# Performance work log

Hardware: AMD Instinct MI355X
Metric: run time of the kernel (lower is better)

Reference implementation:

```python
import jax, jax.numpy as jnp
import numpy as np

HIDDEN = 256


def _lstm_cell(x, h, c, W_ih, W_hh, b_ih, b_hh):
    # torch.nn.LSTMCell: gates ordered [i, f, g, o], gates = x W_ih^T + h W_hh^T + b_ih + b_hh
    gates = x @ W_ih.T + h @ W_hh.T + (b_ih + b_hh)
    i, f, g, o = jnp.split(gates, 4, axis=-1)
    c_new = jax.nn.sigmoid(f) * c + jax.nn.sigmoid(i) * jnp.tanh(g)
    h_new = jax.nn.sigmoid(o) * jnp.tanh(c_new)
    return h_new, c_new


def setup_inputs() -> dict:
    key = jax.random.key(0)
    ks = jax.random.split(key, 16)
    s = 1.0 / np.sqrt(HIDDEN)  # torch LSTMCell init scale
    inp = {
        "tracks": jax.random.normal(ks[0], (256, 512, 2), dtype=jnp.float32),
        "W_ih0": jax.random.uniform(ks[1], (1024, 2), jnp.float32, -s, s),
        "W_hh0": jax.random.uniform(ks[2], (1024, 256), jnp.float32, -s, s),
        "b_ih0": jax.random.uniform(ks[3], (1024,), jnp.float32, -s, s),
        "b_hh0": jax.random.uniform(ks[4], (1024,), jnp.float32, -s, s),
        "W_ih1": jax.random.uniform(ks[5], (1024, 256), jnp.float32, -s, s),
        "W_hh1": jax.random.uniform(ks[6], (1024, 256), jnp.float32, -s, s),
        "b_ih1": jax.random.uniform(ks[7], (1024,), jnp.float32, -s, s),
        "b_hh1": jax.random.uniform(ks[8], (1024,), jnp.float32, -s, s),
        "W_ih2": jax.random.uniform(ks[9], (1024, 256), jnp.float32, -s, s),
        "W_hh2": jax.random.uniform(ks[10], (1024, 256), jnp.float32, -s, s),
        "b_ih2": jax.random.uniform(ks[11], (1024,), jnp.float32, -s, s),
        "b_hh2": jax.random.uniform(ks[12], (1024,), jnp.float32, -s, s),
        "W_pred": jax.random.uniform(ks[13], (2, 256), jnp.float32, -s, s),
        "b_pred": jax.random.uniform(ks[14], (2,), jnp.float32, -s, s),
    }
    return inp


def reference(tracks, W_ih0, W_hh0, b_ih0, b_hh0, W_ih1, W_hh1, b_ih1, b_hh1,
              W_ih2, W_hh2, b_ih2, b_hh2, W_pred, b_pred):
    B = tracks.shape[0]
    layers = [(W_ih0, W_hh0, b_ih0, b_hh0),
              (W_ih1, W_hh1, b_ih1, b_hh1),
              (W_ih2, W_hh2, b_ih2, b_hh2)]
    zeros = jnp.zeros((B, HIDDEN), dtype=tracks.dtype)
    init_carry = tuple((zeros, zeros) for _ in layers)

    def step(carry, x_t):
        new_carry = []
        h = x_t
        for (hc, params) in zip(carry, layers):
            h, c = _lstm_cell(h, hc[0], hc[1], *params)
            new_carry.append((h, c))
        return tuple(new_carry), None

    xs = jnp.swapaxes(tracks, 0, 1)  # [T, B, 2]
    final_carry, _ = jax.lax.scan(step, init_carry, xs)
    h = final_carry[-1][0]  # last layer's final hidden state
    h = jax.nn.elu(h)
    return h @ W_pred.T + b_pred
```

## Files before the change

kernel.cpp:

```cpp
#include <hip/hip_runtime.h>
#include <math.h>

typedef __attribute__((ext_vector_type(4))) float f32x4;
typedef __attribute__((ext_vector_type(4))) int   i32x4;
typedef __attribute__((ext_vector_type(8))) short bfrag8;

#define WRE_LO_OFF 2621440
#define HB_OFF     5242880
#define TAG_OFF    6815744
#define HSTRIDE    65536

#define WROW 264
#define SMEM_BYTES (4 * 64 * WROW * 2)

__device__ __forceinline__ unsigned short f2bf(float f){
  union { float f; unsigned u; } x; x.f = f;
  unsigned r = x.u + 0x7FFFu + ((x.u >> 16) & 1u);
  return (unsigned short)(r >> 16);
}
__device__ __forceinline__ float bf2f(unsigned short s){
  union { unsigned u; float f; } x; x.u = ((unsigned)s) << 16; return x.f;
}
__device__ __forceinline__ float sigf(float x){
  return 1.0f / (1.0f + __expf(-x));
}
__device__ __forceinline__ float tanh_fast(float x){
  x = fminf(fmaxf(x, -15.0f), 15.0f);
  float e = __expf(2.0f * x);
  return (e - 1.0f) / (e + 1.0f);
}

__device__ __forceinline__ i32x4 llc_load_b128(const void* p){
  i32x4 r;
  asm volatile("global_load_dwordx4 %0, %1, off sc0 sc1"
               : "=v"(r) : "v"(p) : "memory");
  return r;
}
__device__ __forceinline__ void llc_store_b16(void* p, unsigned short v){
  unsigned int vv = v;
  asm volatile("global_store_short %0, %1, off sc0 sc1"
               : : "v"(p), "v"(vv) : "memory");
}
__device__ __forceinline__ void wait_vm0(){
  asm volatile("s_waitcnt vmcnt(0)" ::: "memory");
}

__global__ void init_reorder(const float* __restrict__ hh0, const float* __restrict__ ih1,
                             const float* __restrict__ hh1, const float* __restrict__ ih2,
                             const float* __restrict__ hh2,
                             unsigned short* __restrict__ wre_hi,
                             unsigned short* __restrict__ wre_lo){
  int e = blockIdx.x * 256 + threadIdx.x;
  int mat = e >> 18;
  int d   = (e >> 8) & 1023;
  int k   = e & 255;
  int nt = d >> 6, g = (d >> 4) & 3, n = d & 15;
  int src_row = g*256 + nt*16 + n;
  const float* W = (mat==0) ? hh0 : (mat==1) ? ih1 : (mat==2) ? hh1 : (mat==3) ? ih2 : hh2;
  float v = W[src_row*256 + k];
  unsigned short hi = f2bf(v);
  float lo = v - bf2f(hi);
  wre_hi[e] = hi;
  wre_lo[e] = f2bf(lo);
}

__global__ void init_zero(uint4* __restrict__ p, int n16){
  int i = blockIdx.x * 256 + threadIdx.x;
  if (i < n16) p[i] = make_uint4(0u,0u,0u,0u);
}

__global__ void init_tags(unsigned int* __restrict__ tags){
  int i = blockIdx.x * 256 + threadIdx.x;
  if (i < 3072) tags[i] = (unsigned)(i / 768);
}

__global__ void __launch_bounds__(256, 1) lstm_coop(
    const float* __restrict__ tracks,
    const float* __restrict__ wih0,
    const float* __restrict__ bih0, const float* __restrict__ bhh0,
    const float* __restrict__ bih1, const float* __restrict__ bhh1,
    const float* __restrict__ bih2, const float* __restrict__ bhh2,
    const unsigned short* __restrict__ wre_hi, const unsigned short* __restrict__ wre_lo,
    unsigned short* __restrict__ hb, unsigned int* __restrict__ tags);

template<int L>
__device__ __forceinline__ void layer_loop(
    const float* __restrict__ tracks, const float* __restrict__ wih0,
    const float* __restrict__ bihL, const float* __restrict__ bhhL,
    const unsigned short* smem,
    unsigned short* hb, unsigned int* tags,
    int nt, int bt)
{
  const int tid  = threadIdx.x;
  const int w    = tid >> 6, lane = tid & 63;
  const int m    = lane & 15, q = lane >> 4;
  const int b0   = bt * 64, n0 = nt * 16;
  const int G    = bt * 4 + w;

  float bsum[4], wx0[4], wx1[4];
  #pragma unroll
  for (int g = 0; g < 4; ++g){
    int row = g*256 + n0 + m;
    bsum[g] = bihL[row] + bhhL[row];
    if constexpr (L == 0){ wx0[g] = wih0[row*2 + 0]; wx1[g] = wih0[row*2 + 1]; }
  }
  float cst[4] = {0.f, 0.f, 0.f, 0.f};
  const int arow = b0 + 16*w + m;
  const int woff = m*WROW + q*8;
  constexpr int RS = (L == 0) ? 0 : 2;

  for (int t = 0; t < 512; ++t){
    const int pin  = t & 3;
    const int prec = (t + 3) & 3;
    const unsigned expi = (unsigned)(t + 4);
    const unsigned expr = (unsigned)(t + 3);

    unsigned gv = 0u;
    unsigned int* gl = nullptr;
    if constexpr (L < 2){
      gl = tags + ((pin*3 + (L+1))*16 + G)*16;
      if (lane < 16)
        gv = __hip_atomic_load(gl + lane, __ATOMIC_RELAXED, __HIP_MEMORY_SCOPE_AGENT);
    }

    float xv0[4], xv1[4];
    if constexpr (L == 0){
      #pragma unroll
      for (int r = 0; r < 4; ++r){
        const float* px = tracks + (b0 + 16*w + q*4 + r)*1024 + t*2;
        xv0[r] = px[0]; xv1[r] = px[1];
      }
    }

    unsigned int* rcl = tags + ((prec*3 + L)*16 + G)*16;
    unsigned int* inl = nullptr;
    if constexpr (L >= 1) inl = tags + ((pin*3 + (L-1))*16 + G)*16;
    for (;;){
      bool ok = true;
      if constexpr (L >= 1){
        if (lane < 16)
          ok = __hip_atomic_load(inl + lane, __ATOMIC_RELAXED, __HIP_MEMORY_SCOPE_AGENT) >= expi;
        else if (lane < 32)
          ok = __hip_atomic_load(rcl + (lane - 16), __ATOMIC_RELAXED, __HIP_MEMORY_SCOPE_AGENT) >= expr;
      } else {
        if (lane < 16)
          ok = __hip_atomic_load(rcl + lane, __ATOMIC_RELAXED, __HIP_MEMORY_SCOPE_AGENT) >= expr;
      }
      if (__all((int)ok)) break;
    }

    i32x4 arr[8], ari[8];
    {
      const unsigned short* pr = hb + (prec*3 + L)*HSTRIDE + arow*256 + q*8;
      #pragma unroll
      for (int ks = 0; ks < 8; ++ks) arr[ks] = llc_load_b128(pr + ks*32);
      if constexpr (L >= 1){
        const unsigned short* pi = hb + (pin*3 + (L-1))*HSTRIDE + arow*256 + q*8;
        #pragma unroll
        for (int ks = 0; ks < 8; ++ks) ari[ks] = llc_load_b128(pi + ks*32);
      }
    }
    wait_vm0();

    f32x4 acc[4];
    #pragma unroll
    for (int g = 0; g < 4; ++g) acc[g] = (f32x4){0.f,0.f,0.f,0.f};
    {
      const unsigned short* bh = smem + (RS + 0)*64*WROW + woff;
      const unsigned short* bl = smem + (RS + 1)*64*WROW + woff;
      #pragma unroll
      for (int ks = 0; ks < 8; ++ks){
        bfrag8 a = __builtin_bit_cast(bfrag8, arr[ks]);
        #pragma unroll
        for (int g = 0; g < 4; ++g){
          bfrag8 fh = *(const bfrag8*)(bh + g*16*WROW + ks*32);
          bfrag8 fl = *(const bfrag8*)(bl + g*16*WROW + ks*32);
          acc[g] = __builtin_amdgcn_mfma_f32_16x16x32_bf16(a, fh, acc[g], 0, 0, 0);
          acc[g] = __builtin_amdgcn_mfma_f32_16x16x32_bf16(a, fl, acc[g], 0, 0, 0);
        }
      }
    }
    if constexpr (L >= 1){
      const unsigned short* bh = smem + 0*64*WROW + woff;
      const unsigned short* bl = smem + 1*64*WROW + woff;
      #pragma unroll
      for (int ks = 0; ks < 8; ++ks){
        bfrag8 a = __builtin_bit_cast(bfrag8, ari[ks]);
        #pragma unroll
        for (int g = 0; g < 4; ++g){
          bfrag8 fh = *(const bfrag8*)(bh + g*16*WROW + ks*32);
          bfrag8 fl = *(const bfrag8*)(bl + g*16*WROW + ks*32);
          acc[g] = __builtin_amdgcn_mfma_f32_16x16x32_bf16(a, fh, acc[g], 0, 0, 0);
          acc[g] = __builtin_amdgcn_mfma_f32_16x16x32_bf16(a, fl, acc[g], 0, 0, 0);
        }
      }
    }

    if constexpr (L < 2){
      for (;;){
        bool ok = (lane < 16) ? (gv >= (unsigned)t) : true;
        if (__all((int)ok)) break;
        if (lane < 16)
          gv = __hip_atomic_load(gl + lane, __ATOMIC_RELAXED, __HIP_MEMORY_SCOPE_AGENT);
      }
    }

    unsigned short* hout = hb + (pin*3 + L)*HSTRIDE;
    #pragma unroll
    for (int r = 0; r < 4; ++r){
      float xi = 0.f, xf = 0.f, xg = 0.f, xo = 0.f;
      if constexpr (L == 0){
        xi = xv0[r]*wx0[0] + xv1[r]*wx1[0];
        xf = xv0[r]*wx0[1] + xv1[r]*wx1[1];
        xg = xv0[r]*wx0[2] + xv1[r]*wx1[2];
        xo = xv0[r]*wx0[3] + xv1[r]*wx1[3];
      }
      float gi = acc[0][r] + bsum[0] + xi;
      float gf = acc[1][r] + bsum[1] + xf;
      float gg = acc[2][r] + bsum[2] + xg;
      float go = acc[3][r] + bsum[3] + xo;
      float iv = sigf(gi);
      float fv = sigf(gf);
      float gvv = tanh_fast(gg);
      float ov = sigf(go);
      cst[r] = fv * cst[r] + iv * gvv;
      float hv = ov * tanh_fast(cst[r]);
      llc_store_b16(&hout[(b0 + 16*w + q*4 + r)*256 + n0 + m], f2bf(hv));
    }

    wait_vm0();
    if (lane == 0)
      __hip_atomic_store(tags + ((pin*3 + L)*16 + G)*16 + nt, (unsigned)(t + 4),
                         __ATOMIC_RELAXED, __HIP_MEMORY_SCOPE_AGENT);
  }
}

__global__ void __launch_bounds__(256, 1) lstm_coop(
    const float* __restrict__ tracks,
    const float* __restrict__ wih0,
    const float* __restrict__ bih0, const float* __restrict__ bhh0,
    const float* __restrict__ bih1, const float* __restrict__ bhh1,
    const float* __restrict__ bih2, const float* __restrict__ bhh2,
    const unsigned short* __restrict__ wre_hi, const unsigned short* __restrict__ wre_lo,
    unsigned short* __restrict__ hb, unsigned int* __restrict__ tags)
{
  extern __shared__ __align__(16) unsigned short smem[];

  const int tid = threadIdx.x;
  const int l   = blockIdx.x >> 6;
  const int r6  = blockIdx.x & 63;
  const int nt  = r6 & 15, bt = r6 >> 4;

  const int nmats = (l == 0) ? 1 : 2;
  const int gmat0 = (l == 0) ? 0 : (l == 1 ? 1 : 3);
  for (int mi = 0; mi < nmats; ++mi){
    const unsigned short* sh = wre_hi + (gmat0 + mi)*262144 + nt*16384;
    const unsigned short* sl = wre_lo + (gmat0 + mi)*262144 + nt*16384;
    unsigned short* dh = smem + (mi*2 + 0)*64*WROW;
    unsigned short* dl = smem + (mi*2 + 1)*64*WROW;
    for (int c = tid; c < 2048; c += 256){
      int r = c >> 5, off = (c & 31) * 8;
      *(uint4*)(dh + r*WROW + off) = *(const uint4*)(sh + r*256 + off);
      *(uint4*)(dl + r*WROW + off) = *(const uint4*)(sl + r*256 + off);
    }
  }
  __syncthreads();

  if (l == 0)      layer_loop<0>(tracks, wih0, bih0, bhh0, smem, hb, tags, nt, bt);
  else if (l == 1) layer_loop<1>(tracks, wih0, bih1, bhh1, smem, hb, tags, nt, bt);
  else             layer_loop<2>(tracks, wih0, bih2, bhh2, smem, hb, tags, nt, bt);
}

__global__ void head_kernel(const unsigned short* __restrict__ hb,
                            const float* __restrict__ wpred,
                            const float* __restrict__ bpred,
                            float* __restrict__ out){
  const int b = blockIdx.x;
  const int k = threadIdx.x;
  const int idx = 11*HSTRIDE + b*256 + k;
  float h = bf2f(hb[idx]);
  float e = (h > 0.f) ? h : expm1f(h);
  float v0 = e * wpred[k];
  float v1 = e * wpred[256 + k];
  #pragma unroll
  for (int off = 32; off > 0; off >>= 1){
    v0 += __shfl_down(v0, off, 64);
    v1 += __shfl_down(v1, off, 64);
  }
  __shared__ float r0[4], r1[4];
  int wv = threadIdx.x >> 6, ln = threadIdx.x & 63;
  if (ln == 0){ r0[wv] = v0; r1[wv] = v1; }
  __syncthreads();
  if (threadIdx.x == 0){
    out[b*2 + 0] = r0[0] + r0[1] + r0[2] + r0[3] + bpred[0];
    out[b*2 + 1] = r1[0] + r1[1] + r1[2] + r1[3] + bpred[1];
  }
}

extern "C" void kernel_launch(void* const* d_in, const int* in_sizes, int n_in,
                              void* d_out, int out_size, void* d_ws, size_t ws_size,
                              hipStream_t stream) {
  const float* tracks = (const float*)d_in[0];
  const float* wih0   = (const float*)d_in[1];
  const float* whh0   = (const float*)d_in[2];
  const float* bih0   = (const float*)d_in[3];
  const float* bhh0   = (const float*)d_in[4];
  const float* wih1   = (const float*)d_in[5];
  const float* whh1   = (const float*)d_in[6];
  const float* bih1   = (const float*)d_in[7];
  const float* bhh1   = (const float*)d_in[8];
  const float* wih2   = (const float*)d_in[9];
  const float* whh2   = (const float*)d_in[10];
  const float* bih2   = (const float*)d_in[11];
  const float* bhh2   = (const float*)d_in[12];
  const float* wpred  = (const float*)d_in[13];
  const float* bpred  = (const float*)d_in[14];
  float* out = (float*)d_out;

  char* ws = (char*)d_ws;
  unsigned short* wre_hi = (unsigned short*)(ws);
  unsigned short* wre_lo = (unsigned short*)(ws + WRE_LO_OFF);
  unsigned short* hb     = (unsigned short*)(ws + HB_OFF);
  unsigned int*   tags   = (unsigned int*)(ws + TAG_OFF);

  (void)hipFuncSetAttribute((const void*)lstm_coop,
                            hipFuncAttributeMaxDynamicSharedMemorySize, SMEM_BYTES);

  init_reorder<<<5120, 256, 0, stream>>>(whh0, wih1, whh1, wih2, whh2, wre_hi, wre_lo);
  init_zero<<<384, 256, 0, stream>>>((uint4*)(ws + HB_OFF), 98304);
  init_tags<<<12, 256, 0, stream>>>(tags);

  void* args[12];
  args[0]  = (void*)&tracks;
  args[1]  = (void*)&wih0;
  args[2]  = (void*)&bih0;
  args[3]  = (void*)&bhh0;
  args[4]  = (void*)&bih1;
  args[5]  = (void*)&bhh1;
  args[6]  = (void*)&bih2;
  args[7]  = (void*)&bhh2;
  args[8]  = (void*)&wre_hi;
  args[9]  = (void*)&wre_lo;
  args[10] = (void*)&hb;
  args[11] = (void*)&tags;
  hipLaunchCooperativeKernel((const void*)lstm_coop, dim3(192), dim3(256), args,
                             SMEM_BYTES, stream);

  head_kernel<<<256, 256, 0, stream>>>(hb, wpred, bpred, out);
}
```

Measured before the change: 3.902 ms.

## Restructure LSTM wavefront: skewed layer schedule, shadow input GEMM, 2-wave blocks

Replaces the per-timestep tag protocol with a skewed global schedule: layer L runs timestep s-2L. The input-projection GEMM for the next step is computed off the critical path, right after the recurrent step, into a carried accumulator. Each workgroup now has 2 waves, each handling 32 batch rows with two interleaved MFMA chains. Synchronisation uses per-group counters with s_sleep polling, and tags are zeroed together with the h buffers. The aim is to shorten the serial dependency chain per step and raise MFMA ILP, at the cost of a more intricate handshake and fewer waves per CU.

```diff
diff --git a/kernel.cpp b/kernel.cpp
--- a/kernel.cpp
+++ b/kernel.cpp
@@ -43,6 +43,9 @@
 }
 __device__ __forceinline__ void wait_vm0(){
   asm volatile("s_waitcnt vmcnt(0)" ::: "memory");
+}
+__device__ __forceinline__ f32x4 mf(bfrag8 a, bfrag8 b, f32x4 c){
+  return __builtin_amdgcn_mfma_f32_16x16x32_bf16(a, b, c, 0, 0, 0);
 }
 
 __global__ void init_reorder(const float* __restrict__ hh0, const float* __restrict__ ih1,
@@ -69,20 +72,6 @@
   if (i < n16) p[i] = make_uint4(0u,0u,0u,0u);
 }
 
-__global__ void init_tags(unsigned int* __restrict__ tags){
-  int i = blockIdx.x * 256 + threadIdx.x;
-  if (i < 3072) tags[i] = (unsigned)(i / 768);
-}
-
-__global__ void __launch_bounds__(256, 1) lstm_coop(
-    const float* __restrict__ tracks,
-    const float* __restrict__ wih0,
-    const float* __restrict__ bih0, const float* __restrict__ bhh0,
-    const float* __restrict__ bih1, const float* __restrict__ bhh1,
-    const float* __restrict__ bih2, const float* __restrict__ bhh2,
-    const unsigned short* __restrict__ wre_hi, const unsigned short* __restrict__ wre_lo,
-    unsigned short* __restrict__ hb, unsigned int* __restrict__ tags);
-
 template<int L>
 __device__ __forceinline__ void layer_loop(
     const float* __restrict__ tracks, const float* __restrict__ wih0,
@@ -95,147 +84,199 @@
   const int w    = tid >> 6, lane = tid & 63;
   const int m    = lane & 15, q = lane >> 4;
   const int b0   = bt * 64, n0 = nt * 16;
-  const int G    = bt * 4 + w;
-
-  float bsum[4], wx0[4], wx1[4];
+  const int bw   = b0 + 32*w;
+
+  const int gid = L*4 + bt;
+  unsigned int* own = tags + gid*64;
+  unsigned int* upb = (L >= 1) ? (tags + (gid-4)*64) : tags;
+  unsigned int* dnb = (L <= 1) ? (tags + (gid+4)*64) : tags;
+  const int mslot = w*16 + nt;
+  const int sslot = 32 + w*16 + nt;
+
+  float bsum[4], wxa[4], wxb[4];
   #pragma unroll
   for (int g = 0; g < 4; ++g){
     int row = g*256 + n0 + m;
     bsum[g] = bihL[row] + bhhL[row];
-    if constexpr (L == 0){ wx0[g] = wih0[row*2 + 0]; wx1[g] = wih0[row*2 + 1]; }
-  }
-  float cst[4] = {0.f, 0.f, 0.f, 0.f};
-  const int arow = b0 + 16*w + m;
+    if constexpr (L == 0){ wxa[g] = wih0[row*2 + 0]; wxb[g] = wih0[row*2 + 1]; }
+    else { wxa[g] = 0.f; wxb[g] = 0.f; }
+  }
+  float cst[2][4];
+  f32x4 xacc[2][4];
+  #pragma unroll
+  for (int j = 0; j < 2; ++j){
+    #pragma unroll
+    for (int r = 0; r < 4; ++r) cst[j][r] = 0.f;
+    #pragma unroll
+    for (int g = 0; g < 4; ++g) xacc[j][g] = (f32x4){0.f,0.f,0.f,0.f};
+  }
+
   const int woff = m*WROW + q*8;
   constexpr int RS = (L == 0) ? 0 : 2;
 
-  for (int t = 0; t < 512; ++t){
-    const int pin  = t & 3;
-    const int prec = (t + 3) & 3;
-    const unsigned expi = (unsigned)(t + 4);
-    const unsigned expr = (unsigned)(t + 3);
-
-    unsigned gv = 0u;
-    unsigned int* gl = nullptr;
-    if constexpr (L < 2){
-      gl = tags + ((pin*3 + (L+1))*16 + G)*16;
-      if (lane < 16)
-        gv = __hip_atomic_load(gl + lane, __ATOMIC_RELAXED, __HIP_MEMORY_SCOPE_AGENT);
-    }
-
-    float xv0[4], xv1[4];
+  for (int s = 0; s < 516; ++s){
+    const int ph = s - 2*L;
+    const bool mact = (ph >= 0) && (ph < 512);
+
+    float xv0[2][4], xv1[2][4];
     if constexpr (L == 0){
+      if (mact){
+        #pragma unroll
+        for (int j = 0; j < 2; ++j)
+          #pragma unroll
+          for (int r = 0; r < 4; ++r){
+            const float* px = tracks + (bw + 16*j + q*4 + r)*1024 + ph*2;
+            xv0[j][r] = px[0]; xv1[j][r] = px[1];
+          }
+      }
+    }
+
+    if (mact && s > 0){
+      const int tgt = s;
+      for (;;){
+        int v = tgt;
+        if (lane < 32)
+          v = (int)__hip_atomic_load(own + lane, __ATOMIC_RELAXED, __HIP_MEMORY_SCOPE_AGENT);
+        if (__all((int)(v >= tgt))) break;
+        __builtin_amdgcn_s_sleep(1);
+      }
+    }
+
+    if (mact){
+      const int pt = ph & 3, pp = (ph + 3) & 3;
+
+      i32x4 arr[2][8];
+      const unsigned short* pr = hb + (pp*3 + L)*HSTRIDE;
       #pragma unroll
-      for (int r = 0; r < 4; ++r){
-        const float* px = tracks + (b0 + 16*w + q*4 + r)*1024 + t*2;
-        xv0[r] = px[0]; xv1[r] = px[1];
-      }
-    }
-
-    unsigned int* rcl = tags + ((prec*3 + L)*16 + G)*16;
-    unsigned int* inl = nullptr;
-    if constexpr (L >= 1) inl = tags + ((pin*3 + (L-1))*16 + G)*16;
-    for (;;){
-      bool ok = true;
-      if constexpr (L >= 1){
-        if (lane < 16)
-          ok = __hip_atomic_load(inl + lane, __ATOMIC_RELAXED, __HIP_MEMORY_SCOPE_AGENT) >= expi;
-        else if (lane < 32)
-          ok = __hip_atomic_load(rcl + (lane - 16), __ATOMIC_RELAXED, __HIP_MEMORY_SCOPE_AGENT) >= expr;
-      } else {
-        if (lane < 16)
-          ok = __hip_atomic_load(rcl + lane, __ATOMIC_RELAXED, __HIP_MEMORY_SCOPE_AGENT) >= expr;
-      }
-      if (__all((int)ok)) break;
-    }
-
-    i32x4 arr[8], ari[8];
-    {
-      const unsigned short* pr = hb + (prec*3 + L)*HSTRIDE + arow*256 + q*8;
+      for (int j = 0; j < 2; ++j)
+        #pragma unroll
+        for (int ks = 0; ks < 8; ++ks)
+          arr[j][ks] = llc_load_b128(pr + (bw + 16*j + m)*256 + ks*32 + q*8);
+      wait_vm0();
+
+      f32x4 acc[2][4];
       #pragma unroll
-      for (int ks = 0; ks < 8; ++ks) arr[ks] = llc_load_b128(pr + ks*32);
-      if constexpr (L >= 1){
-        const unsigned short* pi = hb + (pin*3 + (L-1))*HSTRIDE + arow*256 + q*8;
-        #pragma unroll
-        for (int ks = 0; ks < 8; ++ks) ari[ks] = llc_load_b128(pi + ks*32);
-      }
-    }
-    wait_vm0();
-
-    f32x4 acc[4];
-    #pragma unroll
-    for (int g = 0; g < 4; ++g) acc[g] = (f32x4){0.f,0.f,0.f,0.f};
-    {
+      for (int j = 0; j < 2; ++j)
+        #pragma unroll
+        for (int g = 0; g < 4; ++g) acc[j][g] = (f32x4){0.f,0.f,0.f,0.f};
+
       const unsigned short* bh = smem + (RS + 0)*64*WROW + woff;
       const unsigned short* bl = smem + (RS + 1)*64*WROW + woff;
       #pragma unroll
       for (int ks = 0; ks < 8; ++ks){
-        bfrag8 a = __builtin_bit_cast(bfrag8, arr[ks]);
+        bfrag8 a0 = __builtin_bit_cast(bfrag8, arr[0][ks]);
+        bfrag8 a1 = __builtin_bit_cast(bfrag8, arr[1][ks]);
         #pragma unroll
         for (int g = 0; g < 4; ++g){
           bfrag8 fh = *(const bfrag8*)(bh + g*16*WROW + ks*32);
           bfrag8 fl = *(const bfrag8*)(bl + g*16*WROW + ks*32);
-          acc[g] = __builtin_amdgcn_mfma_f32_16x16x32_bf16(a, fh, acc[g], 0, 0, 0);
-          acc[g] = __builtin_amdgcn_mfma_f32_16x16x32_bf16(a, fl, acc[g], 0, 0, 0);
+          acc[0][g] = mf(a0, fh, acc[0][g]);
+          acc[1][g] = mf(a1, fh, acc[1][g]);
+          acc[0][g] = mf(a0, fl, acc[0][g]);
+          acc[1][g] = mf(a1, fl, acc[1][g]);
         }
       }
-    }
-    if constexpr (L >= 1){
-      const unsigned short* bh = smem + 0*64*WROW + woff;
-      const unsigned short* bl = smem + 1*64*WROW + woff;
+
+      unsigned short* hout = hb + (pt*3 + L)*HSTRIDE;
       #pragma unroll
-      for (int ks = 0; ks < 8; ++ks){
-        bfrag8 a = __builtin_bit_cast(bfrag8, ari[ks]);
-        #pragma unroll
-        for (int g = 0; g < 4; ++g){
-          bfrag8 fh = *(const bfrag8*)(bh + g*16*WROW + ks*32);
-          bfrag8 fl = *(const bfrag8*)(bl + g*16*WROW + ks*32);
-          acc[g] = __builtin_amdgcn_mfma_f32_16x16x32_bf16(a, fh, acc[g], 0, 0, 0);
-          acc[g] = __builtin_amdgcn_mfma_f32_16x16x32_bf16(a, fl, acc[g], 0, 0, 0);
+      for (int j = 0; j < 2; ++j){
+        #pragma unroll
+        for (int r = 0; r < 4; ++r){
+          float xi, xf, xg, xo;
+          if constexpr (L == 0){
+            xi = xv0[j][r]*wxa[0] + xv1[j][r]*wxb[0];
+            xf = xv0[j][r]*wxa[1] + xv1[j][r]*wxb[1];
+            xg = xv0[j][r]*wxa[2] + xv1[j][r]*wxb[2];
+            xo = xv0[j][r]*wxa[3] + xv1[j][r]*wxb[3];
+          } else {
+            xi = xacc[j][0][r]; xf = xacc[j][1][r];
+            xg = xacc[j][2][r]; xo = xacc[j][3][r];
+          }
+          float gi = acc[j][0][r] + bsum[0] + xi;
+          float gf = acc[j][1][r] + bsum[1] + xf;
+          float gg = acc[j][2][r] + bsum[2] + xg;
+          float go = acc[j][3][r] + bsum[3] + xo;
+          float iv = sigf(gi);
+          float fv = sigf(gf);
+          float gv = tanh_fast(gg);
+          float ov = sigf(go);
+          cst[j][r] = fv * cst[j][r] + iv * gv;
+          float hv = ov * tanh_fast(cst[j][r]);
+          llc_store_b16(&hout[(bw + 16*j + q*4 + r)*256 + n0 + m], f2bf(hv));
         }
       }
-    }
-
-    if constexpr (L < 2){
-      for (;;){
-        bool ok = (lane < 16) ? (gv >= (unsigned)t) : true;
-        if (__all((int)ok)) break;
-        if (lane < 16)
-          gv = __hip_atomic_load(gl + lane, __ATOMIC_RELAXED, __HIP_MEMORY_SCOPE_AGENT);
-      }
-    }
-
-    unsigned short* hout = hb + (pin*3 + L)*HSTRIDE;
-    #pragma unroll
-    for (int r = 0; r < 4; ++r){
-      float xi = 0.f, xf = 0.f, xg = 0.f, xo = 0.f;
-      if constexpr (L == 0){
-        xi = xv0[r]*wx0[0] + xv1[r]*wx1[0];
-        xf = xv0[r]*wx0[1] + xv1[r]*wx1[1];
-        xg = xv0[r]*wx0[2] + xv1[r]*wx1[2];
-        xo = xv0[r]*wx0[3] + xv1[r]*wx1[3];
-      }
-      float gi = acc[0][r] + bsum[0] + xi;
-      float gf = acc[1][r] + bsum[1] + xf;
-      float gg = acc[2][r] + bsum[2] + xg;
-      float go = acc[3][r] + bsum[3] + xo;
-      float iv = sigf(gi);
-      float fv = sigf(gf);
-      float gvv = tanh_fast(gg);
-      float ov = sigf(go);
-      cst[r] = fv * cst[r] + iv * gvv;
-      float hv = ov * tanh_fast(cst[r]);
-      llc_store_b16(&hout[(b0 + 16*w + q*4 + r)*256 + n0 + m], f2bf(hv));
     }
 
     wait_vm0();
     if (lane == 0)
-      __hip_atomic_store(tags + ((pin*3 + L)*16 + G)*16 + nt, (unsigned)(t + 4),
+      __hip_atomic_store(own + mslot, (unsigned)(s + 1),
                          __ATOMIC_RELAXED, __HIP_MEMORY_SCOPE_AGENT);
-  }
-}
-
-__global__ void __launch_bounds__(256, 1) lstm_coop(
+
+    {
+      const int tgtU = s, tgtD = s - 1;
+      const bool needU = (L >= 1) && (tgtU > 0);
+      const bool needD = (L <= 1) && (tgtD > 0);
+      if (needU || needD){
+        for (;;){
+          bool ok = true;
+          if (needU && lane < 32)
+            ok = ((int)__hip_atomic_load(upb + lane, __ATOMIC_RELAXED,
+                                         __HIP_MEMORY_SCOPE_AGENT) >= tgtU);
+          if (needD && lane >= 32)
+            ok = ((int)__hip_atomic_load(dnb + lane, __ATOMIC_RELAXED,
+                                         __HIP_MEMORY_SCOPE_AGENT) >= tgtD);
+          if (__all((int)ok)) break;
+          __builtin_amdgcn_s_sleep(1);
+        }
+      }
+    }
+
+    bool posted_shadow = false;
+    if constexpr (L >= 1){
+      if (ph >= -1 && ph < 511){
+        const int pin = (ph + 1) & 3;
+        i32x4 ash[2][8];
+        const unsigned short* pi = hb + (pin*3 + (L-1))*HSTRIDE;
+        #pragma unroll
+        for (int j = 0; j < 2; ++j)
+          #pragma unroll
+          for (int ks = 0; ks < 8; ++ks)
+            ash[j][ks] = llc_load_b128(pi + (bw + 16*j + m)*256 + ks*32 + q*8);
+        wait_vm0();
+        if (lane == 0)
+          __hip_atomic_store(own + sslot, (unsigned)(s + 1),
+                             __ATOMIC_RELAXED, __HIP_MEMORY_SCOPE_AGENT);
+        posted_shadow = true;
+
+        #pragma unroll
+        for (int j = 0; j < 2; ++j)
+          #pragma unroll
+          for (int g = 0; g < 4; ++g) xacc[j][g] = (f32x4){0.f,0.f,0.f,0.f};
+        const unsigned short* ih = smem + 0*64*WROW + woff;
+        const unsigned short* il = smem + 1*64*WROW + woff;
+        #pragma unroll
+        for (int ks = 0; ks < 8; ++ks){
+          bfrag8 a0 = __builtin_bit_cast(bfrag8, ash[0][ks]);
+          bfrag8 a1 = __builtin_bit_cast(bfrag8, ash[1][ks]);
+          #pragma unroll
+          for (int g = 0; g < 4; ++g){
+            bfrag8 fh = *(const bfrag8*)(ih + g*16*WROW + ks*32);
+            bfrag8 fl = *(const bfrag8*)(il + g*16*WROW + ks*32);
+            xacc[0][g] = mf(a0, fh, xacc[0][g]);
+            xacc[1][g] = mf(a1, fh, xacc[1][g]);
+            xacc[0][g] = mf(a0, fl, xacc[0][g]);
+            xacc[1][g] = mf(a1, fl, xacc[1][g]);
+          }
+        }
+      }
+    }
+    if (!posted_shadow && lane == 0)
+      __hip_atomic_store(own + sslot, (unsigned)(s + 1),
+                         __ATOMIC_RELAXED, __HIP_MEMORY_SCOPE_AGENT);
+  }
+}
+
+__global__ void __launch_bounds__(128, 1) lstm_coop(
     const float* __restrict__ tracks,
     const float* __restrict__ wih0,
     const float* __restrict__ bih0, const float* __restrict__ bhh0,
@@ -258,7 +299,7 @@
     const unsigned short* sl = wre_lo + (gmat0 + mi)*262144 + nt*16384;
     unsigned short* dh = smem + (mi*2 + 0)*64*WROW;
     unsigned short* dl = smem + (mi*2 + 1)*64*WROW;
-    for (int c = tid; c < 2048; c += 256){
+    for (int c = tid; c < 2048; c += 128){
       int r = c >> 5, off = (c & 31) * 8;
       *(uint4*)(dh + r*WROW + off) = *(const uint4*)(sh + r*256 + off);
       *(uint4*)(dl + r*WROW + off) = *(const uint4*)(sl + r*256 + off);
@@ -327,8 +368,7 @@
                             hipFuncAttributeMaxDynamicSharedMemorySize, SMEM_BYTES);
 
   init_reorder<<<5120, 256, 0, stream>>>(whh0, wih1, whh1, wih2, whh2, wre_hi, wre_lo);
-  init_zero<<<384, 256, 0, stream>>>((uint4*)(ws + HB_OFF), 98304);
-  init_tags<<<12, 256, 0, stream>>>(tags);
+  init_zero<<<385, 256, 0, stream>>>((uint4*)(ws + HB_OFF), 98496);
 
   void* args[12];
   args[0]  = (void*)&tracks;
@@ -343,7 +383,7 @@
   args[9]  = (void*)&wre_lo;
   args[10] = (void*)&hb;
   args[11] = (void*)&tags;
-  hipLaunchCooperativeKernel((const void*)lstm_coop, dim3(192), dim3(256), args,
+  hipLaunchCooperativeKernel((const void*)lstm_coop, dim3(192), dim3(128), args,
                              SMEM_BYTES, stream);
 
   head_kernel<<<256, 256, 0, stream>>>(hb, wpred, bpred, out);
```

Measured after the change: 3.965 ms. No clear change (+1.6%).
